# Kernel tuning notes

Hardware: AMD Instinct MI355X
Metric: run time of the kernel (lower is better)

The kernel has to match this reference:

```python
import jax, jax.numpy as jnp
import numpy as np

D_MODEL = 512
D_STATE = 64
N_LAYERS = 6
L_SEQ = 784
BATCH = 64


def _layernorm(x, g, b, eps=1e-5):
    mu = x.mean(-1, keepdims=True)
    var = ((x - mu) ** 2).mean(-1, keepdims=True)
    return (x - mu) * jax.lax.rsqrt(var + eps) * g + b


def _s4d_kernel(log_dt, log_A_real, A_imag, C_re, C_im, L):
    # log_dt: (H,), others: (H, N). Returns real conv kernel (H, L).
    dt = jnp.exp(log_dt)[:, None]                      # (H,1)
    A = -jnp.exp(log_A_real) + 1j * A_imag             # (H,N) complex
    C = C_re + 1j * C_im                               # (H,N)
    dtA = A * dt                                       # (H,N)
    Cd = C * (jnp.exp(dtA) - 1.0) / A                  # ZOH-discretized C
    # Vandermonde: V[h,n,l] = exp(dtA[h,n] * l)
    V = jnp.exp(dtA[:, :, None] * jnp.arange(L, dtype=jnp.float32))  # (H,N,L)
    K = 2.0 * jnp.einsum('hn,hnl->hl', Cd, V).real     # (H,L)
    return K


def _s4_fftconv(u, K, D):
    # u: (B,L,H), K: (H,L), D: (H,)
    L = u.shape[1]
    uf = jnp.fft.rfft(u, 2 * L, axis=1)                # (B, L+1, H)
    kf = jnp.fft.rfft(K.T, 2 * L, axis=0)              # (L+1, H)
    y = jnp.fft.irfft(uf * kf[None], 2 * L, axis=1)[:, :L]
    return y + u * D


def setup_inputs() -> dict:
    key = jax.random.key(0)
    ks = jax.random.split(key, 12)
    H, N, NL = D_MODEL, D_STATE, N_LAYERS
    x = jax.random.normal(ks[0], (BATCH, L_SEQ, 1), dtype=jnp.float32)
    enc_w = jax.random.normal(ks[1], (1, H), dtype=jnp.float32) * 0.5
    enc_b = jnp.zeros((H,), dtype=jnp.float32)
    # S4D-Lin style init, stacked over layers
    log_dt = jnp.tile(
        jax.random.uniform(ks[2], (H,), minval=np.log(0.001), maxval=np.log(0.1)),
        (NL, 1))                                        # (NL,H)
    log_A_real = jnp.full((NL, H, N), jnp.log(0.5), dtype=jnp.float32)
    A_imag = jnp.tile(np.pi * jnp.arange(N, dtype=jnp.float32), (NL, H, 1))
    C_re = jax.random.normal(ks[3], (NL, H, N), dtype=jnp.float32) * (0.5 ** 0.5)
    C_im = jax.random.normal(ks[4], (NL, H, N), dtype=jnp.float32) * (0.5 ** 0.5)
    D = jax.random.normal(ks[5], (NL, H), dtype=jnp.float32)
    ln_g = jnp.ones((NL, H), dtype=jnp.float32)
    ln_b = jnp.zeros((NL, H), dtype=jnp.float32)
    fn_g = jnp.ones((H,), dtype=jnp.float32)
    fn_b = jnp.zeros((H,), dtype=jnp.float32)
    dec_w = jax.random.normal(ks[6], (H, 10), dtype=jnp.float32) / jnp.sqrt(H)
    dec_b = jnp.zeros((10,), dtype=jnp.float32)
    return dict(x=x, enc_w=enc_w, enc_b=enc_b, log_dt=log_dt,
                log_A_real=log_A_real, A_imag=A_imag, C_re=C_re, C_im=C_im,
                D=D, ln_g=ln_g, ln_b=ln_b, fn_g=fn_g, fn_b=fn_b,
                dec_w=dec_w, dec_b=dec_b)


def reference(x, enc_w, enc_b, log_dt, log_A_real, A_imag, C_re, C_im, D,
              ln_g, ln_b, fn_g, fn_b, dec_w, dec_b):
    h = x @ enc_w + enc_b                               # (B,L,H)
    L = h.shape[1]
    for i in range(log_dt.shape[0]):                    # fixed n_layers
        K = _s4d_kernel(log_dt[i], log_A_real[i], A_imag[i], C_re[i], C_im[i], L)
        z = _s4_fftconv(h, K, D[i])                     # S4 output (dropout=eval)
        h = _layernorm(h + z, ln_g[i], ln_b[i])         # residual + LN
    h = _layernorm(h, fn_g, fn_b)
    h = h.mean(axis=1)                                  # mean pool over seq
    return h @ dec_w + dec_b                            # (B,10)
```

## Files before the change

kernel.cpp:

```cpp
#include <hip/hip_runtime.h>
#include <hip/hip_bf16.h>

#define HD 512
#define NST 64
#define NLAY 6
#define LSEQ 784
#define BB 64
#define NKA 848
#define TOFF 800
#define LPADROWS 800
#define KSTR 850
#define CHK2 5
#define NCH 5
#define UTS2 9

typedef unsigned short u16;
typedef short s8v __attribute__((ext_vector_type(8)));
typedef float f16v __attribute__((ext_vector_type(16)));
typedef u16  u4h __attribute__((ext_vector_type(4)));
typedef u16  u8h __attribute__((ext_vector_type(8)));

__device__ __forceinline__ unsigned f2b(float f)
{
    unsigned u = __builtin_bit_cast(unsigned, f);
    return (u + 0x7FFFu + ((u >> 16) & 1u)) >> 16;
}
__device__ __forceinline__ float b2f16(u16 v)
{
    unsigned u = ((unsigned)v) << 16;
    return __builtin_bit_cast(float, u);
}
__device__ __forceinline__ unsigned pkbf(float lo, float hi)
{
    unsigned r;
    asm("v_cvt_pk_bf16_f32 %0, %1, %2" : "=v"(r) : "v"(lo), "v"(hi));
    return r;
}

__global__ void precompute_k(const float* __restrict__ log_dt,
                             const float* __restrict__ log_A_real,
                             const float* __restrict__ A_imag,
                             const float* __restrict__ C_re,
                             const float* __restrict__ C_im,
                             float* __restrict__ lamr, float* __restrict__ lami,
                             float* __restrict__ dtr,  float* __restrict__ dti,
                             float* __restrict__ c2r,  float* __restrict__ c2i)
{
    int t = blockIdx.x * 256 + threadIdx.x;
    if (t >= NLAY * HD * NST) return;
    int ih = t >> 6;
    float dt  = expf(log_dt[ih]);
    float are = -expf(log_A_real[t]);
    float aim = A_imag[t];
    float dr = are * dt, di = aim * dt;
    float er = expf(dr);
    float sn, cs; __sincosf(di, &sn, &cs);
    float lr = er * cs, li = er * sn;
    float e1r = lr - 1.0f, e1i = li;
    float den = are * are + aim * aim;
    float qr = (e1r * are + e1i * aim) / den;
    float qi = (e1i * are - e1r * aim) / den;
    float crv = C_re[t], civ = C_im[t];
    lamr[t] = lr; lami[t] = li; dtr[t] = dr; dti[t] = di;
    c2r[t] = 2.0f * (crv * qr - civ * qi);
    c2i[t] = 2.0f * (crv * qi + civ * qr);
}

__global__ void kq_k(const float* __restrict__ lamr, const float* __restrict__ lami,
                     const float* __restrict__ dtr,  const float* __restrict__ dti,
                     const float* __restrict__ c2r,  const float* __restrict__ c2i,
                     u16* __restrict__ KA)
{
    int t = blockIdx.x * 256 + threadIdx.x;
    int q  = t & 3;
    int u  = t >> 2;
    int dc = u % 49;
    int ih = u / 49;
    int d0 = dc * 16;
    float acc[16];
#pragma unroll
    for (int k = 0; k < 16; k++) acc[k] = 0.f;
    int base = ih * 64 + q * 16;
    for (int n = 0; n < 16; n += 4) {
        float lr[4], li[4], cr[4], ci[4], pr[4], pi[4];
#pragma unroll
        for (int j = 0; j < 4; j++) {
            int qq = base + n + j;
            lr[j] = lamr[qq]; li[j] = lami[qq];
            float dr = dtr[qq], di = dti[qq];
            cr[j] = c2r[qq]; ci[j] = c2i[qq];
            float e = __expf(dr * (float)d0);
            float sn, cs; __sincosf(di * (float)d0, &sn, &cs);
            pr[j] = e * cs; pi[j] = e * sn;
        }
#pragma unroll
        for (int k = 0; k < 16; k++) {
#pragma unroll
            for (int j = 0; j < 4; j++) {
                acc[k] = fmaf(cr[j], pr[j], fmaf(-ci[j], pi[j], acc[k]));
                float nr = pr[j] * lr[j] - pi[j] * li[j];
                pi[j] = fmaf(pr[j], li[j], pi[j] * lr[j]);
                pr[j] = nr;
            }
        }
    }
#pragma unroll
    for (int k = 0; k < 16; k++) {
        acc[k] += __shfl_xor(acc[k], 1);
        acc[k] += __shfl_xor(acc[k], 2);
    }
    if (q == 0) {
        u16* kap = KA + (size_t)ih * NKA;
#pragma unroll
        for (int k = 0; k < 16; k++)
            kap[TOFF - (d0 + k)] = (u16)f2b(acc[k]);
        if (dc == 0)  for (int z = TOFF + 1; z < NKA; z++) kap[z] = 0;
        if (dc == 48) for (int z = 0; z < TOFF - 783; z++) kap[z] = 0;
    }
}

__global__ void xt_k(const float* __restrict__ x, float* __restrict__ xT)
{
    int t = blockIdx.x * 256 + threadIdx.x;
    int l = t >> 6, b = t & 63;
    xT[t] = x[b * LSEQ + l];
}

__global__ void encoder_k(const float* __restrict__ xT, const float* __restrict__ ew,
                          const float* __restrict__ eb, u16* __restrict__ Vb)
{
    int g = blockIdx.x * 256 + threadIdx.x;
    int bo = g & 7;
    int h  = (g >> 3) & 511;
    int l  = g >> 12;
    uint4* dst = (uint4*)&Vb[((size_t)l * HD + h) * BB + 8 * bo];
    if (l >= LSEQ) { *dst = (uint4){0, 0, 0, 0}; return; }
    const float4* xp = (const float4*)&xT[l * BB + 8 * bo];
    float4 a0 = xp[0], a1 = xp[1];
    float w = ew[h], bb = eb[h];
    unsigned p0 = pkbf(fmaf(a0.x, w, bb), fmaf(a0.y, w, bb));
    unsigned p1 = pkbf(fmaf(a0.z, w, bb), fmaf(a0.w, w, bb));
    unsigned p2 = pkbf(fmaf(a1.x, w, bb), fmaf(a1.y, w, bb));
    unsigned p3 = pkbf(fmaf(a1.z, w, bb), fmaf(a1.w, w, bb));
    *dst = (uint4){p0, p1, p2, p3};
}

__global__ __launch_bounds__(128, 4)
void conv_k(const u16* __restrict__ Vb, u16* __restrict__ V2,
            const u16* __restrict__ KA, const float* __restrict__ Dvec)
{
    __shared__ __align__(16) u16 KR[6816];
    __shared__ __align__(16) unsigned UT[2][2][64 * UTS2];

    const int thr = threadIdx.x;
    const int h   = blockIdx.x & 511;
    const int c   = NCH - 1 - (blockIdx.x >> 9);
    const int w   = thr >> 6;
    const int lane = thr & 63;
    const int n2 = lane & 31;
    const int qp = lane >> 5;
    const int JTN = 5 * c + 5;

    const u16* kap = KA + (size_t)h * NKA;
    {
        int s = thr & 7, ch = thr >> 3;
        int i0 = ch * 53;
        int i1 = (i0 + 53 < NKA) ? (i0 + 53) : NKA;
        u16* kr = KR + KSTR * s + ((8 - s) & 7);
        for (int i = i0; i < i1; i++) kr[i] = kap[i];
    }

    const int jj = thr >> 4;
    const int bq = thr & 15;

    auto LOAD16 = [&](int j0, u4h& r0, u4h& r1) {
        int j = j0 + 2 * jj;
        const u16* p = &Vb[((size_t)j * HD + h) * BB + 4 * bq];
        r0 = *(const u4h*)p;
        r1 = *(const u4h*)(p + (size_t)HD * BB);
    };
    auto WRITE16 = [&](unsigned* up, u4h r0, u4h r1) {
#pragma unroll
        for (int i = 0; i < 4; i++)
            up[(4 * bq + i) * UTS2 + jj] = (unsigned)r0[i] | ((unsigned)r1[i] << 16);
    };

    {
        u4h t0, t1;
        LOAD16(0, t0, t1);
        WRITE16(&UT[0][0][0], t0, t1);
        LOAD16(16, t0, t1);
        WRITE16(&UT[0][1][0], t0, t1);
    }
    __syncthreads();

    f16v acc[CHK2];
#pragma unroll
    for (int i = 0; i < CHK2; i++)
#pragma unroll
        for (int r = 0; r < 16; r++) acc[i][r] = 0.f;

    const float dcoef = 1.0f + Dvec[h];

    const int s = lane & 7;
    const u16* krb = KR + KSTR * s + ((8 - s) & 7)
                     + (TOFF - 160 * c) + 8 * qp - n2;
    const int uoff = (32 * w + n2) * UTS2 + 4 * qp;
    const unsigned* bA0 = &UT[0][0][uoff];
    const unsigned* bB0 = &UT[0][1][uoff];
    const unsigned* bA1 = &UT[1][0][uoff];
    const unsigned* bB1 = &UT[1][1][uoff];

    for (int J = 0; J < JTN; ++J) {
        u4h ra0, ra1, rb0, rb1;
        const bool more = (J + 1) < JTN;
        if (more) {
            LOAD16(32 * (J + 1),      ra0, ra1);
            LOAD16(32 * (J + 1) + 16, rb0, rb1);
        }

        const unsigned* bbA = (J & 1) ? bA1 : bA0;
        const unsigned* bbB = (J & 1) ? bB1 : bB0;
        union { unsigned u[4]; s8v v; } buA, buB;
        buA.u[0] = bbA[0]; buA.u[1] = bbA[1]; buA.u[2] = bbA[2]; buA.u[3] = bbA[3];
        buB.u[0] = bbB[0]; buB.u[1] = bbB[1]; buB.u[2] = bbB[2]; buB.u[3] = bbB[3];

        const u16* ap0 = krb + 32 * J;
#pragma unroll
        for (int lt = 0; lt < CHK2; ++lt) {
            const int lim = 10 * c + 2 * lt + 1;
            if (2 * J <= lim) {
                s8v av = *(const s8v*)__builtin_assume_aligned(ap0 - 32 * lt, 16);
                acc[lt] = __builtin_amdgcn_mfma_f32_32x32x16_bf16(av, buA.v, acc[lt], 0, 0, 0);
            }
            if (2 * J + 1 <= lim) {
                s8v av = *(const s8v*)__builtin_assume_aligned(ap0 + 16 - 32 * lt, 16);
                acc[lt] = __builtin_amdgcn_mfma_f32_32x32x16_bf16(av, buB.v, acc[lt], 0, 0, 0);
            }
        }
        if (more) {
            WRITE16(&UT[(J & 1) ^ 1][0][0], ra0, ra1);
            WRITE16(&UT[(J & 1) ^ 1][1][0], rb0, rb1);
        }
        __syncthreads();
    }

#pragma unroll
    for (int lt = 0; lt < CHK2; ++lt) {
        const int l0 = 32 * (5 * c + lt) + 4 * qp;
#pragma unroll
        for (int r = 0; r < 16; ++r) {
            int l = l0 + (r & 3) + 8 * (r >> 2);
            size_t a = ((size_t)l * HD + h) * BB + 32 * w + n2;
            V2[a] = (u16)f2b(fmaf(dcoef, b2f16(Vb[a]), acc[lt][r]));
        }
    }
}

__global__ __launch_bounds__(512)
void lnT_k(const u16* __restrict__ src, u16* __restrict__ dst,
           const float* __restrict__ gp, const float* __restrict__ bp)
{
    __shared__ float redS[8][64], redQ[8][64];
    __shared__ float mus[64], rss[64];
    __shared__ float gs[512], bs[512];
    const int thr = threadIdx.x;
    const int lane = thr & 63;
    const int wv = thr >> 6;
    const int bo = thr & 7;
    const int hg = thr >> 3;
    const size_t l = blockIdx.x;
    gs[thr] = gp[thr]; bs[thr] = bp[thr];

    const u16* sp = &src[(l * HD + hg * 8) * BB + 8 * bo];
    float v[64];
    float s[8] = {0, 0, 0, 0, 0, 0, 0, 0};
    float q[8] = {0, 0, 0, 0, 0, 0, 0, 0};
#pragma unroll
    for (int k = 0; k < 8; k++) {
        u8h r = *(const u8h*)(sp + (size_t)k * BB);
#pragma unroll
        for (int i = 0; i < 8; i++) {
            float x = b2f16(r[i]);
            v[k * 8 + i] = x;
            s[i] += x;
            q[i] = fmaf(x, x, q[i]);
        }
    }
#pragma unroll
    for (int i = 0; i < 8; i++) {
        s[i] += __shfl_xor(s[i], 8);  q[i] += __shfl_xor(q[i], 8);
        s[i] += __shfl_xor(s[i], 16); q[i] += __shfl_xor(q[i], 16);
        s[i] += __shfl_xor(s[i], 32); q[i] += __shfl_xor(q[i], 32);
    }
    if (lane < 8) {
#pragma unroll
        for (int i = 0; i < 8; i++) {
            redS[wv][8 * lane + i] = s[i];
            redQ[wv][8 * lane + i] = q[i];
        }
    }
    __syncthreads();
    if (thr < 64) {
        float ts = 0.f, tq = 0.f;
#pragma unroll
        for (int g = 0; g < 8; g++) { ts += redS[g][thr]; tq += redQ[g][thr]; }
        float mu = ts * (1.0f / HD);
        mus[thr] = mu;
        rss[thr] = rsqrtf(tq * (1.0f / HD) - mu * mu + 1e-5f);
    }
    __syncthreads();
    float mu[8], rs[8];
#pragma unroll
    for (int i = 0; i < 8; i++) { mu[i] = mus[8 * bo + i]; rs[i] = rss[8 * bo + i]; }
    u16* dp = &dst[(l * HD + hg * 8) * BB + 8 * bo];
#pragma unroll
    for (int k = 0; k < 8; k++) {
        float g = gs[hg * 8 + k], bb = bs[hg * 8 + k];
        float y[8];
#pragma unroll
        for (int i = 0; i < 8; i++)
            y[i] = fmaf((v[k * 8 + i] - mu[i]) * rs[i], g, bb);
        uint4 pkt = {pkbf(y[0], y[1]), pkbf(y[2], y[3]),
                     pkbf(y[4], y[5]), pkbf(y[6], y[7])};
        *(uint4*)(dp + (size_t)k * BB) = pkt;
    }
}

__global__ __launch_bounds__(512)
void lnT2s_k(const u16* __restrict__ src, u16* __restrict__ dst,
             const float* __restrict__ g5p, const float* __restrict__ b5p,
             const float* __restrict__ gp, const float* __restrict__ bp)
{
    __shared__ float redS[8][64], redQ[8][64];
    __shared__ float mu1s[64], rs1s[64], mu2s[64], rs2s[64];
    __shared__ float gs[512], bs[512];
    const int thr = threadIdx.x;
    const int lane = thr & 63;
    const int wv = thr >> 6;
    const int bo = thr & 7;
    const int hg = thr >> 3;
    const size_t l = blockIdx.x;
    gs[thr] = gp[thr]; bs[thr] = bp[thr];

    const u16* sp = &src[(l * HD + (size_t)hg * 8) * BB + 8 * bo];
    float v[64];
    float s[8] = {0, 0, 0, 0, 0, 0, 0, 0};
    float q[8] = {0, 0, 0, 0, 0, 0, 0, 0};
#pragma unroll
    for (int k = 0; k < 8; k++) {
        u8h r = *(const u8h*)(sp + (size_t)k * BB);
#pragma unroll
        for (int i = 0; i < 8; i++) {
            float x = b2f16(r[i]);
            v[k * 8 + i] = x;
            s[i] += x;
            q[i] = fmaf(x, x, q[i]);
        }
    }
#pragma unroll
    for (int i = 0; i < 8; i++) {
        s[i] += __shfl_xor(s[i], 8);  q[i] += __shfl_xor(q[i], 8);
        s[i] += __shfl_xor(s[i], 16); q[i] += __shfl_xor(q[i], 16);
        s[i] += __shfl_xor(s[i], 32); q[i] += __shfl_xor(q[i], 32);
    }
    if (lane < 8) {
#pragma unroll
        for (int i = 0; i < 8; i++) {
            redS[wv][8 * lane + i] = s[i];
            redQ[wv][8 * lane + i] = q[i];
        }
    }
    __syncthreads();
    if (thr < 64) {
        float ts = 0.f, tq = 0.f;
#pragma unroll
        for (int g = 0; g < 8; g++) { ts += redS[g][thr]; tq += redQ[g][thr]; }
        float mu = ts * (1.0f / HD);
        mu1s[thr] = mu;
        rs1s[thr] = rsqrtf(tq * (1.0f / HD) - mu * mu + 1e-5f);
    }
    __syncthreads();
    float mu1[8], rs1[8];
#pragma unroll
    for (int i = 0; i < 8; i++) { mu1[i] = mu1s[8 * bo + i]; rs1[i] = rs1s[8 * bo + i]; }

    float s2[8] = {0, 0, 0, 0, 0, 0, 0, 0};
    float q2[8] = {0, 0, 0, 0, 0, 0, 0, 0};
#pragma unroll
    for (int k = 0; k < 8; k++) {
        float g5 = g5p[hg * 8 + k], b5 = b5p[hg * 8 + k];
#pragma unroll
        for (int i = 0; i < 8; i++) {
            float x = fmaf((v[k * 8 + i] - mu1[i]) * rs1[i], g5, b5);
            v[k * 8 + i] = x;
            s2[i] += x;
            q2[i] = fmaf(x, x, q2[i]);
        }
    }
#pragma unroll
    for (int i = 0; i < 8; i++) {
        s2[i] += __shfl_xor(s2[i], 8);  q2[i] += __shfl_xor(q2[i], 8);
        s2[i] += __shfl_xor(s2[i], 16); q2[i] += __shfl_xor(q2[i], 16);
        s2[i] += __shfl_xor(s2[i], 32); q2[i] += __shfl_xor(q2[i], 32);
    }
    __syncthreads();
    if (lane < 8) {
#pragma unroll
        for (int i = 0; i < 8; i++) {
            redS[wv][8 * lane + i] = s2[i];
            redQ[wv][8 * lane + i] = q2[i];
        }
    }
    __syncthreads();
    if (thr < 64) {
        float ts = 0.f, tq = 0.f;
#pragma unroll
        for (int g = 0; g < 8; g++) { ts += redS[g][thr]; tq += redQ[g][thr]; }
        float mu = ts * (1.0f / HD);
        mu2s[thr] = mu;
        rs2s[thr] = rsqrtf(tq * (1.0f / HD) - mu * mu + 1e-5f);
    }
    __syncthreads();
    float mu2[8], rs2[8];
#pragma unroll
    for (int i = 0; i < 8; i++) { mu2[i] = mu2s[8 * bo + i]; rs2[i] = rs2s[8 * bo + i]; }
    u16* dp = &dst[(l * HD + (size_t)hg * 8) * BB + 8 * bo];
#pragma unroll
    for (int k = 0; k < 8; k++) {
        float g = gs[hg * 8 + k], bb = bs[hg * 8 + k];
        float y[8];
#pragma unroll
        for (int i = 0; i < 8; i++)
            y[i] = fmaf((v[k * 8 + i] - mu2[i]) * rs2[i], g, bb);
        uint4 pkt = {pkbf(y[0], y[1]), pkbf(y[2], y[3]),
                     pkbf(y[4], y[5]), pkbf(y[6], y[7])};
        *(uint4*)(dp + (size_t)k * BB) = pkt;
    }
}

__global__ __launch_bounds__(256)
void pool2_k(const u16* __restrict__ Vb, float* __restrict__ PO2)
{
    const int cb = blockIdx.x & 15;
    const int lg = blockIdx.x >> 4;
    const int off = cb * 2048 + threadIdx.x * 8;
    const u16* p = Vb + (size_t)(lg * 49) * (HD * BB) + off;
    float s[8] = {0, 0, 0, 0, 0, 0, 0, 0};
    for (int l = 0; l < 49; l++) {
        u8h r = *(const u8h*)p;
        p += HD * BB;
#pragma unroll
        for (int i = 0; i < 8; i++) s[i] += b2f16(r[i]);
    }
    float* q = PO2 + (size_t)lg * (HD * BB) + off;
    *(float4*)q       = (float4){s[0], s[1], s[2], s[3]};
    *(float4*)(q + 4) = (float4){s[4], s[5], s[6], s[7]};
}

__global__ void poolr_k(const float* __restrict__ PO2, float* __restrict__ PO)
{
    int t = blockIdx.x * 256 + threadIdx.x;
    float s = 0.f;
#pragma unroll
    for (int g = 0; g < 16; g++) s += PO2[(size_t)g * (HD * BB) + t];
    PO[t] = s * (1.0f / LSEQ);
}

__global__ void dec_k(const float* __restrict__ PO, const float* __restrict__ w,
                      const float* __restrict__ bias, float* __restrict__ out)
{
    int t = blockIdx.x * 256 + threadIdx.x;
    if (t >= BB * 10) return;
    int cc = t % 10, b = t / 10;
    float acc = bias[cc];
    for (int hh = 0; hh < HD; hh++)
        acc = fmaf(PO[hh * BB + b], w[hh * 10 + cc], acc);
    out[t] = acc;
}

extern "C" void kernel_launch(void* const* d_in, const int* in_sizes, int n_in,
                              void* d_out, int out_size, void* d_ws, size_t ws_size,
                              hipStream_t stream)
{
    const float* x   = (const float*)d_in[0];
    const float* ew  = (const float*)d_in[1];
    const float* eb  = (const float*)d_in[2];
    const float* ldt = (const float*)d_in[3];
    const float* lar = (const float*)d_in[4];
    const float* aim = (const float*)d_in[5];
    const float* cre = (const float*)d_in[6];
    const float* cim = (const float*)d_in[7];
    const float* Dp  = (const float*)d_in[8];
    const float* lng = (const float*)d_in[9];
    const float* lnb = (const float*)d_in[10];
    const float* fng = (const float*)d_in[11];
    const float* fnb = (const float*)d_in[12];
    const float* dw  = (const float*)d_in[13];
    const float* db  = (const float*)d_in[14];
    float* out = (float*)d_out;

    const size_t SZB = (size_t)BB * LPADROWS * HD;
    const size_t PP  = (size_t)NLAY * HD * NST;
    u16*   Vb  = (u16*)d_ws;
    u16*   V2  = Vb + SZB;
    float* PAR = (float*)(V2 + SZB);
    float* lamr = PAR,        * lami = PAR + PP;
    float* dtr  = PAR + 2*PP, * dti  = PAR + 3*PP;
    float* c2r  = PAR + 4*PP, * c2i  = PAR + 5*PP;
    u16* KA = (u16*)(PAR + 6 * PP);
    float* PO = PAR + 6 * PP + (NLAY * HD * NKA) / 2;
    float* xT = PO + BB * HD;
    float* PO2 = xT + LSEQ * BB;

    precompute_k<<<(NLAY * HD * NST + 255) / 256, 256, 0, stream>>>(
        ldt, lar, aim, cre, cim, lamr, lami, dtr, dti, c2r, c2i);
    kq_k<<<(NLAY * HD * 49 * 4) / 256, 256, 0, stream>>>(
        lamr, lami, dtr, dti, c2r, c2i, KA);
    xt_k<<<(LSEQ * BB) / 256, 256, 0, stream>>>(x, xT);
    encoder_k<<<(LPADROWS * HD * 8) / 256, 256, 0, stream>>>(xT, ew, eb, Vb);

    for (int i = 0; i < NLAY - 1; i++) {
        conv_k<<<512 * NCH, 128, 0, stream>>>(
            Vb, V2, KA + (size_t)i * HD * NKA, Dp + i * HD);
        lnT_k<<<LSEQ, 512, 0, stream>>>(V2, Vb, lng + i * HD, lnb + i * HD);
    }
    conv_k<<<512 * NCH, 128, 0, stream>>>(
        Vb, V2, KA + (size_t)5 * HD * NKA, Dp + 5 * HD);
    lnT2s_k<<<LSEQ, 512, 0, stream>>>(V2, Vb, lng + 5 * HD, lnb + 5 * HD, fng, fnb);

    pool2_k<<<256, 256, 0, stream>>>(Vb, PO2);
    poolr_k<<<(HD * BB) / 256, 256, 0, stream>>>(PO2, PO);
    dec_k<<<(BB * 10 + 255) / 256, 256, 0, stream>>>(PO, dw, db, out);
}
```

Measured before the change: 541.3 us.

## Double conv_k block size and split output tiles across wave pairs

New measurement: 553.2 us. 2.2% more time.

```diff
diff --git a/kernel.cpp b/kernel.cpp
--- a/kernel.cpp
+++ b/kernel.cpp
@@ -10,7 +10,6 @@
 #define TOFF 800
 #define LPADROWS 800
 #define KSTR 850
-#define CHK2 5
 #define NCH 5
 #define UTS2 9
 
@@ -145,7 +144,7 @@
     *dst = (uint4){p0, p1, p2, p3};
 }
 
-__global__ __launch_bounds__(128, 4)
+__global__ __launch_bounds__(256, 4)
 void conv_k(const u16* __restrict__ Vb, u16* __restrict__ V2,
             const u16* __restrict__ KA, const float* __restrict__ Dvec)
 {
@@ -155,7 +154,9 @@
     const int thr = threadIdx.x;
     const int h   = blockIdx.x & 511;
     const int c   = NCH - 1 - (blockIdx.x >> 9);
-    const int w   = thr >> 6;
+    const int ww  = thr >> 6;
+    const int w   = ww & 1;
+    const int p   = ww >> 1;
     const int lane = thr & 63;
     const int n2 = lane & 31;
     const int qp = lane >> 5;
@@ -164,8 +165,8 @@
     const u16* kap = KA + (size_t)h * NKA;
     {
         int s = thr & 7, ch = thr >> 3;
-        int i0 = ch * 53;
-        int i1 = (i0 + 53 < NKA) ? (i0 + 53) : NKA;
+        int i0 = ch * 27;
+        int i1 = (i0 + 27 < NKA) ? (i0 + 27) : NKA;
         u16* kr = KR + KSTR * s + ((8 - s) & 7);
         for (int i = i0; i < i1; i++) kr[i] = kap[i];
     }
@@ -173,30 +174,30 @@
     const int jj = thr >> 4;
     const int bq = thr & 15;
 
-    auto LOAD16 = [&](int j0, u4h& r0, u4h& r1) {
+    auto LOAD32 = [&](int j0, u4h& r0, u4h& r1) {
         int j = j0 + 2 * jj;
-        const u16* p = &Vb[((size_t)j * HD + h) * BB + 4 * bq];
-        r0 = *(const u4h*)p;
-        r1 = *(const u4h*)(p + (size_t)HD * BB);
+        const u16* pp = &Vb[((size_t)j * HD + h) * BB + 4 * bq];
+        r0 = *(const u4h*)pp;
+        r1 = *(const u4h*)(pp + (size_t)HD * BB);
     };
-    auto WRITE16 = [&](unsigned* up, u4h r0, u4h r1) {
+    auto WRITE32 = [&](int buf, u4h r0, u4h r1) {
+        unsigned* up = &UT[buf][jj >> 3][0];
+        const int jl = jj & 7;
 #pragma unroll
         for (int i = 0; i < 4; i++)
-            up[(4 * bq + i) * UTS2 + jj] = (unsigned)r0[i] | ((unsigned)r1[i] << 16);
+            up[(4 * bq + i) * UTS2 + jl] = (unsigned)r0[i] | ((unsigned)r1[i] << 16);
     };
 
     {
         u4h t0, t1;
-        LOAD16(0, t0, t1);
-        WRITE16(&UT[0][0][0], t0, t1);
-        LOAD16(16, t0, t1);
-        WRITE16(&UT[0][1][0], t0, t1);
-    }
-    __syncthreads();
-
-    f16v acc[CHK2];
-#pragma unroll
-    for (int i = 0; i < CHK2; i++)
+        LOAD32(0, t0, t1);
+        WRITE32(0, t0, t1);
+    }
+    __syncthreads();
+
+    f16v acc[3];
+#pragma unroll
+    for (int i = 0; i < 3; i++)
 #pragma unroll
         for (int r = 0; r < 16; r++) acc[i][r] = 0.f;
 
@@ -212,12 +213,9 @@
     const unsigned* bB1 = &UT[1][1][uoff];
 
     for (int J = 0; J < JTN; ++J) {
-        u4h ra0, ra1, rb0, rb1;
+        u4h ra0, ra1;
         const bool more = (J + 1) < JTN;
-        if (more) {
-            LOAD16(32 * (J + 1),      ra0, ra1);
-            LOAD16(32 * (J + 1) + 16, rb0, rb1);
-        }
+        if (more) LOAD32(32 * (J + 1), ra0, ra1);
 
         const unsigned* bbA = (J & 1) ? bA1 : bA0;
         const unsigned* bbB = (J & 1) ? bB1 : bB0;
@@ -227,32 +225,35 @@
 
         const u16* ap0 = krb + 32 * J;
 #pragma unroll
-        for (int lt = 0; lt < CHK2; ++lt) {
-            const int lim = 10 * c + 2 * lt + 1;
-            if (2 * J <= lim) {
-                s8v av = *(const s8v*)__builtin_assume_aligned(ap0 - 32 * lt, 16);
-                acc[lt] = __builtin_amdgcn_mfma_f32_32x32x16_bf16(av, buA.v, acc[lt], 0, 0, 0);
+        for (int lt = 0; lt < 3; ++lt) {
+            const int ti = 2 * lt + p;
+            if (ti <= 4) {
+                const int lim = 10 * c + 2 * ti + 1;
+                if (2 * J <= lim) {
+                    s8v av = *(const s8v*)__builtin_assume_aligned(ap0 - 32 * ti, 16);
+                    acc[lt] = __builtin_amdgcn_mfma_f32_32x32x16_bf16(av, buA.v, acc[lt], 0, 0, 0);
+                }
+                if (2 * J + 1 <= lim) {
+                    s8v av = *(const s8v*)__builtin_assume_aligned(ap0 + 16 - 32 * ti, 16);
+                    acc[lt] = __builtin_amdgcn_mfma_f32_32x32x16_bf16(av, buB.v, acc[lt], 0, 0, 0);
+                }
             }
-            if (2 * J + 1 <= lim) {
-                s8v av = *(const s8v*)__builtin_assume_aligned(ap0 + 16 - 32 * lt, 16);
-                acc[lt] = __builtin_amdgcn_mfma_f32_32x32x16_bf16(av, buB.v, acc[lt], 0, 0, 0);
+        }
+        if (more) WRITE32((J & 1) ^ 1, ra0, ra1);
+        __syncthreads();
+    }
+
+#pragma unroll
+    for (int lt = 0; lt < 3; ++lt) {
+        const int ti = 2 * lt + p;
+        if (ti <= 4) {
+            const int l0 = 32 * (5 * c + ti) + 4 * qp;
+#pragma unroll
+            for (int r = 0; r < 16; ++r) {
+                int l = l0 + (r & 3) + 8 * (r >> 2);
+                size_t a = ((size_t)l * HD + h) * BB + 32 * w + n2;
+                V2[a] = (u16)f2b(fmaf(dcoef, b2f16(Vb[a]), acc[lt][r]));
             }
-        }
-        if (more) {
-            WRITE16(&UT[(J & 1) ^ 1][0][0], ra0, ra1);
-            WRITE16(&UT[(J & 1) ^ 1][1][0], rb0, rb1);
-        }
-        __syncthreads();
-    }
-
-#pragma unroll
-    for (int lt = 0; lt < CHK2; ++lt) {
-        const int l0 = 32 * (5 * c + lt) + 4 * qp;
-#pragma unroll
-        for (int r = 0; r < 16; ++r) {
-            int l = l0 + (r & 3) + 8 * (r >> 2);
-            size_t a = ((size_t)l * HD + h) * BB + 32 * w + n2;
-            V2[a] = (u16)f2b(fmaf(dcoef, b2f16(Vb[a]), acc[lt][r]));
         }
     }
 }
@@ -521,11 +522,11 @@
     encoder_k<<<(LPADROWS * HD * 8) / 256, 256, 0, stream>>>(xT, ew, eb, Vb);
 
     for (int i = 0; i < NLAY - 1; i++) {
-        conv_k<<<512 * NCH, 128, 0, stream>>>(
+        conv_k<<<512 * NCH, 256, 0, stream>>>(
             Vb, V2, KA + (size_t)i * HD * NKA, Dp + i * HD);
         lnT_k<<<LSEQ, 512, 0, stream>>>(V2, Vb, lng + i * HD, lnb + i * HD);
     }
-    conv_k<<<512 * NCH, 128, 0, stream>>>(
+    conv_k<<<512 * NCH, 256, 0, stream>>>(
         Vb, V2, KA + (size_t)5 * HD * NKA, Dp + 5 * HD);
     lnT2s_k<<<LSEQ, 512, 0, stream>>>(V2, Vb, lng + 5 * HD, lnb + 5 * HD, fng, fnb);
 
```
